# Optimization experiments

Measured on AMD Instinct MI355X. Metric: run time of the kernel, lower is better.

The kernel has to match this reference:

```python
import jax, jax.numpy as jnp
import numpy as np

SR = 44100.0  # sample_rate from init_kwargs


def _alpha(tau_ms):
    # Eq. (10): alpha = exp(-1 / (tau_s * fs)), tau clamped to [0.1, 1000] ms
    tau_s = jnp.clip(tau_ms, 0.1, 1000.0) / 1000.0
    return jnp.exp(-1.0 / (tau_s * SR))


def _env(x, alpha, attack):
    # Nonlinear envelope follower (Eqs. 9-10).
    # attack=True  -> smooth attack (when |x| rising), instant decay
    # attack=False -> smooth decay  (when |x| falling), instant attack
    xa = jnp.abs(x)
    xs = jnp.moveaxis(xa, -1, 0)  # [T, B, C]
    y0 = jnp.zeros(xa.shape[:-1], xa.dtype)  # [B, C]

    def step(y_prev, xn):
        cond = (xn > y_prev) if attack else (xn < y_prev)
        y_curr = jnp.where(cond, (1.0 - alpha) * xn + alpha * y_prev, xn)
        return y_curr, y_curr

    _, ys = jax.lax.scan(step, y0, xs)
    return jnp.moveaxis(ys, 0, -1)  # [B, C, T]


def _db_to_amp(db):
    return jnp.power(10.0, db / 20.0)


def reference(x, tauAtc, tauDtc, nu, dBregDelta):
    # Temporal Contrast Enhancement (Weger et al., ICAD 2019, Eqs. 12-14).
    # high_pass_filter is the identity in the source, so sh = x.
    alpha_d = _alpha(jnp.clip(tauDtc, 1.0, 100.0))
    alpha_a = _alpha(jnp.clip(tauAtc, 1.0, 100.0))
    et_d = _env(x, alpha_d, attack=False)      # envd(sh)
    et_a = _env(et_d, alpha_a, attack=True)    # enva(et_d)
    nu_amp = _db_to_amp(jnp.clip(nu, -60.0, 0.0))
    et = jnp.maximum(et_d - et_a - nu_amp, 0.0)
    et_env = _env(et, alpha_d, attack=False)   # envd(et)
    reg = _db_to_amp(jnp.clip(dBregDelta, -120.0, -60.0))
    modulation = et / (et_env + reg)
    return x * modulation


def setup_inputs() -> dict:
    key = jax.random.key(0)
    x = jax.random.normal(key, (8, 32, 88200), dtype=jnp.float32)  # [B, C, T]
    return {
        "x": x,
        "tauAtc": jnp.float32(3.0),
        "tauDtc": jnp.float32(7.0),
        "nu": jnp.float32(-40.0),
        "dBregDelta": jnp.float32(-96.0),
    }
```

## Files before the change

### kernel.cpp

```cpp
#include <hip/hip_runtime.h>
#include <cmath>


typedef float f32x4 __attribute__((ext_vector_type(4)));

static constexpr int   kT  = 88200;
static constexpr float kSR = 44100.0f;

static constexpr int S       = 40;
static constexpr int NC      = kT / S;
static constexpr int PADS    = S + 4;
static constexpr int CHT     = 256;
static constexpr int NT      = (NC + CHT - 1) / CHT;
static constexpr int TAILC   = NC - CHT * (NT - 1);
static constexpr int F4C     = S / 4;
static constexpr int TILE_F4 = CHT * F4C;
static constexpr int TAIL_F4 = TAILC * F4C;
static constexpr int BUF_F   = CHT * PADS;

struct EnvP { float ad, bd, aa, ba, nuamp, reg; };

__device__ __forceinline__ EnvP make_params(const float* tauA, const float* tauD,
                                            const float* nu, const float* dbreg) {
  EnvP p;
  float td = fminf(fmaxf(tauD[0], 1.0f), 100.0f);
  td = fminf(fmaxf(td, 0.1f), 1000.0f) * 0.001f;
  float ta = fminf(fmaxf(tauA[0], 1.0f), 100.0f);
  ta = fminf(fmaxf(ta, 0.1f), 1000.0f) * 0.001f;
  p.ad = expf(-1.0f / (td * kSR));
  p.aa = expf(-1.0f / (ta * kSR));
  p.bd = 1.0f - p.ad;
  p.ba = 1.0f - p.aa;
  p.nuamp = exp10f(fminf(fmaxf(nu[0],    -60.0f),   0.0f) * 0.05f);
  p.reg   = exp10f(fminf(fmaxf(dbreg[0], -120.0f), -60.0f) * 0.05f);
  return p;
}

template <int MODE>
__device__ __forceinline__ void sweep(const float* __restrict__ xs,
                                      float* __restrict__ os,
                                      const EnvP& p,
                                      float* __restrict__ buf0,
                                      float* __restrict__ buf1,
                                      float* __restrict__ Ac, float* __restrict__ Bc,
                                      const float* __restrict__ Ydl,
                                      const float* __restrict__ Yal,
                                      const float* __restrict__ Yel,
                                      int t) {
  f32x4 r0, r1, r2, r3, r4, r5, r6, r7, r8, r9;
  const f32x4* xg4 = reinterpret_cast<const f32x4*>(xs);

#define LD_TILE(TILE)                                                        \
  do {                                                                       \
    const int nf4_ = ((TILE) == NT - 1) ? TAIL_F4 : TILE_F4;                 \
    const f32x4* xg_ = xg4 + (size_t)(TILE) * TILE_F4;                       \
    int i0_ = t;                                                             \
    r0 = xg_[i0_ < nf4_ ? i0_ : 0];  i0_ += 256;                             \
    r1 = xg_[i0_ < nf4_ ? i0_ : 0];  i0_ += 256;                             \
    r2 = xg_[i0_ < nf4_ ? i0_ : 0];  i0_ += 256;                             \
    r3 = xg_[i0_ < nf4_ ? i0_ : 0];  i0_ += 256;                             \
    r4 = xg_[i0_ < nf4_ ? i0_ : 0];  i0_ += 256;                             \
    r5 = xg_[i0_ < nf4_ ? i0_ : 0];  i0_ += 256;                             \
    r6 = xg_[i0_ < nf4_ ? i0_ : 0];  i0_ += 256;                             \
    r7 = xg_[i0_ < nf4_ ? i0_ : 0];  i0_ += 256;                             \
    r8 = xg_[i0_ < nf4_ ? i0_ : 0];  i0_ += 256;                             \
    r9 = xg_[i0_ < nf4_ ? i0_ : 0];                                          \
  } while (0)

#define WR_TILE(BUF)                                                         \
  do {                                                                       \
    float* b_ = (BUF);                                                       \
    int i0_ = t, ch_, of_;                                                   \
    ch_ = i0_ / F4C; of_ = (i0_ - ch_ * F4C) * 4;                            \
    *reinterpret_cast<f32x4*>(&b_[ch_ * PADS + of_]) = r0;  i0_ += 256;      \
    ch_ = i0_ / F4C; of_ = (i0_ - ch_ * F4C) * 4;                            \
    *reinterpret_cast<f32x4*>(&b_[ch_ * PADS + of_]) = r1;  i0_ += 256;      \
    ch_ = i0_ / F4C; of_ = (i0_ - ch_ * F4C) * 4;                            \
    *reinterpret_cast<f32x4*>(&b_[ch_ * PADS + of_]) = r2;  i0_ += 256;      \
    ch_ = i0_ / F4C; of_ = (i0_ - ch_ * F4C) * 4;                            \
    *reinterpret_cast<f32x4*>(&b_[ch_ * PADS + of_]) = r3;  i0_ += 256;      \
    ch_ = i0_ / F4C; of_ = (i0_ - ch_ * F4C) * 4;                            \
    *reinterpret_cast<f32x4*>(&b_[ch_ * PADS + of_]) = r4;  i0_ += 256;      \
    ch_ = i0_ / F4C; of_ = (i0_ - ch_ * F4C) * 4;                            \
    *reinterpret_cast<f32x4*>(&b_[ch_ * PADS + of_]) = r5;  i0_ += 256;      \
    ch_ = i0_ / F4C; of_ = (i0_ - ch_ * F4C) * 4;                            \
    *reinterpret_cast<f32x4*>(&b_[ch_ * PADS + of_]) = r6;  i0_ += 256;      \
    ch_ = i0_ / F4C; of_ = (i0_ - ch_ * F4C) * 4;                            \
    *reinterpret_cast<f32x4*>(&b_[ch_ * PADS + of_]) = r7;  i0_ += 256;      \
    ch_ = i0_ / F4C; of_ = (i0_ - ch_ * F4C) * 4;                            \
    *reinterpret_cast<f32x4*>(&b_[ch_ * PADS + of_]) = r8;  i0_ += 256;      \
    ch_ = i0_ / F4C; of_ = (i0_ - ch_ * F4C) * 4;                            \
    *reinterpret_cast<f32x4*>(&b_[ch_ * PADS + of_]) = r9;                   \
  } while (0)

  LD_TILE(0);
  WR_TILE(buf0);
  __syncthreads();
  int cur = 0;
  for (int it = 0; it < NT; ++it) {
    const bool pf = (it + 1 < NT);
    if (pf) LD_TILE(it + 1);
    __builtin_amdgcn_sched_barrier(0);
    float* bc = cur ? buf1 : buf0;
    float* bn = cur ? buf0 : buf1;
    const int c = it * CHT + t;
    if (c < NC) {
      float* my = &bc[t * PADS];
      if (MODE == 0) {
        float A = -INFINITY, B = 0.0f;
#pragma unroll 2
        for (int i = 0; i < F4C; ++i) {
          f32x4 v = *reinterpret_cast<const f32x4*>(&my[4 * i]);
#pragma unroll
          for (int j = 0; j < 4; ++j) {
            float xa = fabsf(v[j]);
            float bx = p.bd * xa;
            A = fmaxf(xa, fmaf(p.ad, A, bx));
            B = fmaf(p.ad, B, bx);
          }
        }
        Ac[c] = A; Bc[c] = B;
      } else if (MODE == 1) {
        float yd = Ydl[c];
        float A = INFINITY, B = 0.0f;
#pragma unroll 2
        for (int i = 0; i < F4C; ++i) {
          f32x4 v = *reinterpret_cast<const f32x4*>(&my[4 * i]);
#pragma unroll
          for (int j = 0; j < 4; ++j) {
            float xa = fabsf(v[j]);
            yd = fmaxf(xa, fmaf(p.ad, yd, p.bd * xa));
            float by = p.ba * yd;
            A = fminf(yd, fmaf(p.aa, A, by));
            B = fmaf(p.aa, B, by);
          }
        }
        Ac[c] = A; Bc[c] = B;
      } else if (MODE == 2) {
        float yd = Ydl[c], ya = Yal[c];
        float A = -INFINITY, B = 0.0f;
#pragma unroll 2
        for (int i = 0; i < F4C; ++i) {
          f32x4 v = *reinterpret_cast<const f32x4*>(&my[4 * i]);
#pragma unroll
          for (int j = 0; j < 4; ++j) {
            float xa = fabsf(v[j]);
            yd = fmaxf(xa, fmaf(p.ad, yd, p.bd * xa));
            ya = fminf(yd, fmaf(p.aa, ya, p.ba * yd));
            float et = fmaxf((yd - ya) - p.nuamp, 0.0f);
            float bx = p.bd * et;
            A = fmaxf(et, fmaf(p.ad, A, bx));
            B = fmaf(p.ad, B, bx);
          }
        }
        Ac[c] = A; Bc[c] = B;
      } else {
        float yd = Ydl[c], ya = Yal[c], ye = Yel[c];
#pragma unroll 2
        for (int i = 0; i < F4C; ++i) {
          f32x4 v = *reinterpret_cast<const f32x4*>(&my[4 * i]);
          f32x4 oo;
#pragma unroll
          for (int j = 0; j < 4; ++j) {
            float xa = fabsf(v[j]);
            yd = fmaxf(xa, fmaf(p.ad, yd, p.bd * xa));
            ya = fminf(yd, fmaf(p.aa, ya, p.ba * yd));
            float et = fmaxf((yd - ya) - p.nuamp, 0.0f);
            ye = fmaxf(et, fmaf(p.ad, ye, p.bd * et));
            oo[j] = v[j] * (et / (ye + p.reg));
          }
          *reinterpret_cast<f32x4*>(&my[4 * i]) = oo;
        }
      }
    }
    if (MODE == 3) {
      __syncthreads();
      f32x4* og = reinterpret_cast<f32x4*>(os) + (size_t)it * TILE_F4;
      const int nf4 = pf ? TILE_F4 : TAIL_F4;
#pragma unroll
      for (int i = 0; i < F4C; ++i) {
        int idx = t + i * 256;
        if (idx < nf4) {
          int chunk = idx / F4C;
          int off   = (idx - chunk * F4C) * 4;
          f32x4 v = *reinterpret_cast<const f32x4*>(&bc[chunk * PADS + off]);
          __builtin_nontemporal_store(v, &og[idx]);
        }
      }
    }
    if (pf) WR_TILE(bn);
    __syncthreads();
    cur ^= 1;
  }
#undef LD_TILE
#undef WR_TILE
}

template <int ATTACK>
__device__ __forceinline__ void scan_lds(const float* __restrict__ Ac,
                                         const float* __restrict__ Bc,
                                         float* __restrict__ Y,
                                         const EnvP& p,
                                         float* __restrict__ sbuf, int t) {
  constexpr int CPT = (NC + 255) / 256;
  const float alpha = ATTACK ? p.aa : p.ad;
  const float ID_A  = ATTACK ? INFINITY : -INFINITY;
  const float gS = powf(alpha, (float)S);

  float ca[CPT], cb[CPT];
  float a = ID_A, b = 0.0f, g = 1.0f;
#pragma unroll
  for (int k = 0; k < CPT; ++k) {
    int c = t * CPT + k;
    if (c < NC) { ca[k] = Ac[c]; cb[k] = Bc[c]; }
    else        { ca[k] = ID_A;  cb[k] = 0.0f; }
    float cg = (c < NC) ? gS : 1.0f;
    float na = ATTACK ? fminf(ca[k], fmaf(cg, a, cb[k]))
                      : fmaxf(ca[k], fmaf(cg, a, cb[k]));
    b = fmaf(cg, b, cb[k]);
    g = cg * g;
    a = na;
  }

  float* sA = sbuf; float* sB = sbuf + 256; float* sG = sbuf + 512;
  sA[t] = a; sB[t] = b; sG[t] = g;
  __syncthreads();
#pragma unroll
  for (int d = 1; d < 256; d <<= 1) {
    float pa = 0.0f, pb = 0.0f, pg = 0.0f;
    if (t >= d) { pa = sA[t - d]; pb = sB[t - d]; pg = sG[t - d]; }
    __syncthreads();
    if (t >= d) {
      float na = ATTACK ? fminf(a, fmaf(g, pa, b)) : fmaxf(a, fmaf(g, pa, b));
      b = fmaf(g, pb, b);
      g = g * pg;
      a = na;
      sA[t] = a; sB[t] = b; sG[t] = g;
    }
    __syncthreads();
  }

  float ea, eb;
  if (t == 0) { ea = ID_A; eb = 0.0f; }
  else        { ea = sA[t - 1]; eb = sB[t - 1]; }

#pragma unroll
  for (int k = 0; k < CPT; ++k) {
    int c = t * CPT + k;
    if (c >= NC) break;
    Y[c] = ATTACK ? fminf(ea, eb) : fmaxf(ea, eb);
    float na = ATTACK ? fminf(ca[k], fmaf(gS, ea, cb[k]))
                      : fmaxf(ca[k], fmaf(gS, ea, cb[k]));
    eb = fmaf(gS, eb, cb[k]);
    ea = na;
  }
}

__global__
__attribute__((amdgpu_flat_work_group_size(256, 256), amdgpu_waves_per_eu(1, 1)))
void k_one(const float* __restrict__ x,
           const float* tauA, const float* tauD,
           const float* nu, const float* dbreg,
           float* __restrict__ out) {
  extern __shared__ float lds[];
  float* buf0 = lds;
  float* buf1 = lds + BUF_F;
  float* Ac   = lds + 2 * BUF_F;
  float* Bc   = Ac + NC;
  float* Yd   = Bc + NC;
  float* Ya   = Yd + NC;
  float* Ye   = Ya + NC;
  const int t = threadIdx.x;
  const float* xs = x   + (size_t)blockIdx.x * kT;
  float*       os = out + (size_t)blockIdx.x * kT;
  EnvP p = make_params(tauA, tauD, nu, dbreg);

  sweep<0>(xs, nullptr, p, buf0, buf1, Ac, Bc, nullptr, nullptr, nullptr, t);
  scan_lds<0>(Ac, Bc, Yd, p, buf0, t);
  __syncthreads();
  sweep<1>(xs, nullptr, p, buf0, buf1, Ac, Bc, Yd, nullptr, nullptr, t);
  scan_lds<1>(Ac, Bc, Ya, p, buf0, t);
  __syncthreads();
  sweep<2>(xs, nullptr, p, buf0, buf1, Ac, Bc, Yd, Ya, nullptr, t);
  scan_lds<0>(Ac, Bc, Ye, p, buf0, t);
  __syncthreads();
  sweep<3>(xs, os, p, buf0, buf1, Ac, Bc, Yd, Ya, Ye, t);
}

template <int FS, int MODE>
__global__ __launch_bounds__(256)
void k_pass(const float* __restrict__ x,
            const float* tauA, const float* tauD,
            const float* nu, const float* dbreg,
            const float* __restrict__ FYd, const float* __restrict__ FYa,
            const float* __restrict__ FYe,
            float* __restrict__ O0, float* __restrict__ O1) {
  constexpr int FP = FS + 4;
  __shared__ float lds[256 * FP];
  const int t   = threadIdx.x;
  const int blk = blockIdx.x;
  const size_t tileBase = (size_t)blk * (256 * FS);
  const float4* xg = reinterpret_cast<const float4*>(x + tileBase);
#pragma unroll
  for (int i = 0; i < FS / 4; ++i) {
    int idx = t + i * 256;
    float4 v = xg[idx];
    int chunk = (idx * 4) / FS;
    int off   = idx * 4 - chunk * FS;
    *reinterpret_cast<float4*>(&lds[chunk * FP + off]) = v;
  }
  __syncthreads();
  EnvP p = make_params(tauA, tauD, nu, dbreg);
  const int gchunk = blk * 256 + t;
  float* my = &lds[t * FP];
  if (MODE == 0) {
    float A = -INFINITY, B = 0.0f;
#pragma unroll 2
    for (int i = 0; i < FS / 4; ++i) {
      float4 v = *reinterpret_cast<const float4*>(&my[4 * i]);
      float vv[4] = {v.x, v.y, v.z, v.w};
#pragma unroll
      for (int j = 0; j < 4; ++j) {
        float xa = fabsf(vv[j]);
        float bx = p.bd * xa;
        A = fmaxf(xa, fmaf(p.ad, A, bx));
        B = fmaf(p.ad, B, bx);
      }
    }
    O0[gchunk] = A; O1[gchunk] = B;
  } else if (MODE == 1) {
    float yd = FYd[gchunk];
    float A = INFINITY, B = 0.0f;
#pragma unroll 2
    for (int i = 0; i < FS / 4; ++i) {
      float4 v = *reinterpret_cast<const float4*>(&my[4 * i]);
      float vv[4] = {v.x, v.y, v.z, v.w};
#pragma unroll
      for (int j = 0; j < 4; ++j) {
        float xa = fabsf(vv[j]);
        yd = fmaxf(xa, fmaf(p.ad, yd, p.bd * xa));
        float by = p.ba * yd;
        A = fminf(yd, fmaf(p.aa, A, by));
        B = fmaf(p.aa, B, by);
      }
    }
    O0[gchunk] = A; O1[gchunk] = B;
  } else if (MODE == 2) {
    float yd = FYd[gchunk], ya = FYa[gchunk];
    float A = -INFINITY, B = 0.0f;
#pragma unroll 2
    for (int i = 0; i < FS / 4; ++i) {
      float4 v = *reinterpret_cast<const float4*>(&my[4 * i]);
      float vv[4] = {v.x, v.y, v.z, v.w};
#pragma unroll
      for (int j = 0; j < 4; ++j) {
        float xa = fabsf(vv[j]);
        yd = fmaxf(xa, fmaf(p.ad, yd, p.bd * xa));
        ya = fminf(yd, fmaf(p.aa, ya, p.ba * yd));
        float et = fmaxf((yd - ya) - p.nuamp, 0.0f);
        float bx = p.bd * et;
        A = fmaxf(et, fmaf(p.ad, A, bx));
        B = fmaf(p.ad, B, bx);
      }
    }
    O0[gchunk] = A; O1[gchunk] = B;
  } else {
    float yd = FYd[gchunk], ya = FYa[gchunk], ye = FYe[gchunk];
#pragma unroll 2
    for (int i = 0; i < FS / 4; ++i) {
      float4 v = *reinterpret_cast<const float4*>(&my[4 * i]);
      float vv[4] = {v.x, v.y, v.z, v.w};
      float oo[4];
#pragma unroll
      for (int j = 0; j < 4; ++j) {
        float xa = fabsf(vv[j]);
        yd = fmaxf(xa, fmaf(p.ad, yd, p.bd * xa));
        ya = fminf(yd, fmaf(p.aa, ya, p.ba * yd));
        float et = fmaxf((yd - ya) - p.nuamp, 0.0f);
        ye = fmaxf(et, fmaf(p.ad, ye, p.bd * et));
        oo[j] = vv[j] * (et / (ye + p.reg));
      }
      *reinterpret_cast<float4*>(&my[4 * i]) = make_float4(oo[0], oo[1], oo[2], oo[3]);
    }
    __syncthreads();
    float4* og = reinterpret_cast<float4*>(O0 + tileBase);
#pragma unroll
    for (int i = 0; i < FS / 4; ++i) {
      int idx = t + i * 256;
      int chunk = (idx * 4) / FS;
      int off   = idx * 4 - chunk * FS;
      og[idx] = *reinterpret_cast<const float4*>(&lds[chunk * FP + off]);
    }
  }
}

template <int FS, int ATTACK>
__global__ __launch_bounds__(256)
void k_scan(const float* __restrict__ A, const float* __restrict__ B,
            float* __restrict__ Y,
            const float* tauA, const float* tauD,
            const float* nu, const float* dbreg) {
  constexpr int FNC = kT / FS;
  constexpr int CPT = (FNC + 255) / 256;
  EnvP p = make_params(tauA, tauD, nu, dbreg);
  const float alpha = ATTACK ? p.aa : p.ad;
  const float ID_A  = ATTACK ? INFINITY : -INFINITY;
  int s = blockIdx.x, t = threadIdx.x;
  long base = (long)s * FNC;
  float gS = powf(alpha, (float)FS);

  float ca[CPT], cb[CPT];
  float a = ID_A, b = 0.0f, g = 1.0f;
#pragma unroll
  for (int k = 0; k < CPT; ++k) {
    int c = t * CPT + k;
    if (c < FNC) { ca[k] = A[base + c]; cb[k] = B[base + c]; }
    else         { ca[k] = ID_A;        cb[k] = 0.0f; }
    float cg = (c < FNC) ? gS : 1.0f;
    float na = ATTACK ? fminf(ca[k], fmaf(cg, a, cb[k]))
                      : fmaxf(ca[k], fmaf(cg, a, cb[k]));
    b = fmaf(cg, b, cb[k]);
    g = cg * g;
    a = na;
  }

  __shared__ float sA[256], sB[256], sG[256];
  sA[t] = a; sB[t] = b; sG[t] = g;
  __syncthreads();
#pragma unroll
  for (int d = 1; d < 256; d <<= 1) {
    float pa = 0.0f, pb = 0.0f, pg = 0.0f;
    if (t >= d) { pa = sA[t - d]; pb = sB[t - d]; pg = sG[t - d]; }
    __syncthreads();
    if (t >= d) {
      float na = ATTACK ? fminf(a, fmaf(g, pa, b)) : fmaxf(a, fmaf(g, pa, b));
      b = fmaf(g, pb, b);
      g = g * pg;
      a = na;
      sA[t] = a; sB[t] = b; sG[t] = g;
    }
    __syncthreads();
  }

  float ea, eb;
  if (t == 0) { ea = ID_A; eb = 0.0f; }
  else        { ea = sA[t - 1]; eb = sB[t - 1]; }

#pragma unroll
  for (int k = 0; k < CPT; ++k) {
    int c = t * CPT + k;
    if (c >= FNC) break;
    Y[base + c] = ATTACK ? fminf(ea, eb) : fmaxf(ea, eb);
    float na = ATTACK ? fminf(ca[k], fmaf(gS, ea, cb[k]))
                      : fmaxf(ca[k], fmaf(gS, ea, cb[k]));
    eb = fmaf(gS, eb, cb[k]);
    ea = na;
  }
}

template <int FS>
static void run_pipeline(const float* x, const float* tauA, const float* tauD,
                         const float* nu, const float* dbreg, float* out,
                         float* wsf, int nseries, hipStream_t stream) {
  const int nc  = kT / FS;
  const int nch = nseries * nc;
  float* A   = wsf;
  float* B   = wsf + (size_t)nch;
  float* FYd = wsf + (size_t)2 * nch;
  float* FYa = wsf + (size_t)3 * nch;
  float* FYe = wsf + (size_t)4 * nch;
  const int grid = nch / 256;

  k_pass<FS, 0><<<grid, 256, 0, stream>>>(x, tauA, tauD, nu, dbreg, nullptr, nullptr, nullptr, A, B);
  k_scan<FS, 0><<<nseries, 256, 0, stream>>>(A, B, FYd, tauA, tauD, nu, dbreg);
  k_pass<FS, 1><<<grid, 256, 0, stream>>>(x, tauA, tauD, nu, dbreg, FYd, nullptr, nullptr, A, B);
  k_scan<FS, 1><<<nseries, 256, 0, stream>>>(A, B, FYa, tauA, tauD, nu, dbreg);
  k_pass<FS, 2><<<grid, 256, 0, stream>>>(x, tauA, tauD, nu, dbreg, FYd, FYa, nullptr, A, B);
  k_scan<FS, 0><<<nseries, 256, 0, stream>>>(A, B, FYe, tauA, tauD, nu, dbreg);
  k_pass<FS, 3><<<grid, 256, 0, stream>>>(x, tauA, tauD, nu, dbreg, FYd, FYa, FYe, out, nullptr);
}

extern "C" void kernel_launch(void* const* d_in, const int* in_sizes, int n_in,
                              void* d_out, int out_size, void* d_ws, size_t ws_size,
                              hipStream_t stream) {
  const float* x     = (const float*)d_in[0];
  const float* tauA  = (const float*)d_in[1];
  const float* tauD  = (const float*)d_in[2];
  const float* nu    = (const float*)d_in[3];
  const float* dbreg = (const float*)d_in[4];
  float* out = (float*)d_out;
  float* wsf = (float*)d_ws;
  const int nseries = in_sizes[0] / kT;

  constexpr size_t LDSZ = (size_t)(2 * BUF_F + 5 * NC) * sizeof(float);

  static int fusedOK = -1;
  if (fusedOK < 0) {
    hipFuncSetAttribute(reinterpret_cast<const void*>(&k_one),
                        hipFuncAttributeMaxDynamicSharedMemorySize, (int)LDSZ);
    (void)hipGetLastError();
    fusedOK = 1;
  }

  if (fusedOK == 1) {
    k_one<<<nseries, 256, LDSZ, stream>>>(x, tauA, tauD, nu, dbreg, out);
    if (hipGetLastError() == hipSuccess) return;
    fusedOK = 0;
  }

  auto fits = [&](int FS) {
    return (size_t)5 * nseries * (kT / FS) * sizeof(float) <= ws_size;
  };
  if      (fits(40))  run_pipeline<40 >(x, tauA, tauD, nu, dbreg, out, wsf, nseries, stream);
  else if (fits(56))  run_pipeline<56 >(x, tauA, tauD, nu, dbreg, out, wsf, nseries, stream);
  else if (fits(72))  run_pipeline<72 >(x, tauA, tauD, nu, dbreg, out, wsf, nseries, stream);
  else                run_pipeline<120>(x, tauA, tauD, nu, dbreg, out, wsf, nseries, stream);
}
```

Measured before the change: 219.0 us.

## Use 512-thread blocks with 24-sample chunks and move carry arrays to global

```diff
diff --git a/kernel.cpp b/kernel.cpp
--- a/kernel.cpp
+++ b/kernel.cpp
@@ -7,16 +7,16 @@
 static constexpr int   kT  = 88200;
 static constexpr float kSR = 44100.0f;
 
-static constexpr int S       = 40;
-static constexpr int NC      = kT / S;
-static constexpr int PADS    = S + 4;
-static constexpr int CHT     = 256;
-static constexpr int NT      = (NC + CHT - 1) / CHT;
-static constexpr int TAILC   = NC - CHT * (NT - 1);
-static constexpr int F4C     = S / 4;
-static constexpr int TILE_F4 = CHT * F4C;
-static constexpr int TAIL_F4 = TAILC * F4C;
-static constexpr int BUF_F   = CHT * PADS;
+static constexpr int FS_      = 24;
+static constexpr int FNC_     = kT / FS_;
+static constexpr int FPADS    = FS_ + 4;
+static constexpr int FTH      = 512;
+static constexpr int FNT      = (FNC_ + FTH - 1) / FTH;
+static constexpr int FTAILC   = FNC_ - FTH * (FNT - 1);
+static constexpr int FF4C     = FS_ / 4;
+static constexpr int FTILE_F4 = FTH * FF4C;
+static constexpr int FTAIL_F4 = FTAILC * FF4C;
+static constexpr int FBUF_F   = FTH * FPADS;
 
 struct EnvP { float ad, bd, aa, ba, nuamp, reg; };
 
@@ -47,69 +47,57 @@
                                       const float* __restrict__ Yal,
                                       const float* __restrict__ Yel,
                                       int t) {
-  f32x4 r0, r1, r2, r3, r4, r5, r6, r7, r8, r9;
+  f32x4 r0, r1, r2, r3, r4, r5;
   const f32x4* xg4 = reinterpret_cast<const f32x4*>(xs);
 
 #define LD_TILE(TILE)                                                        \
   do {                                                                       \
-    const int nf4_ = ((TILE) == NT - 1) ? TAIL_F4 : TILE_F4;                 \
-    const f32x4* xg_ = xg4 + (size_t)(TILE) * TILE_F4;                       \
+    const int nf4_ = ((TILE) == FNT - 1) ? FTAIL_F4 : FTILE_F4;              \
+    const f32x4* xg_ = xg4 + (size_t)(TILE) * FTILE_F4;                      \
     int i0_ = t;                                                             \
-    r0 = xg_[i0_ < nf4_ ? i0_ : 0];  i0_ += 256;                             \
-    r1 = xg_[i0_ < nf4_ ? i0_ : 0];  i0_ += 256;                             \
-    r2 = xg_[i0_ < nf4_ ? i0_ : 0];  i0_ += 256;                             \
-    r3 = xg_[i0_ < nf4_ ? i0_ : 0];  i0_ += 256;                             \
-    r4 = xg_[i0_ < nf4_ ? i0_ : 0];  i0_ += 256;                             \
-    r5 = xg_[i0_ < nf4_ ? i0_ : 0];  i0_ += 256;                             \
-    r6 = xg_[i0_ < nf4_ ? i0_ : 0];  i0_ += 256;                             \
-    r7 = xg_[i0_ < nf4_ ? i0_ : 0];  i0_ += 256;                             \
-    r8 = xg_[i0_ < nf4_ ? i0_ : 0];  i0_ += 256;                             \
-    r9 = xg_[i0_ < nf4_ ? i0_ : 0];                                          \
+    r0 = xg_[i0_ < nf4_ ? i0_ : 0];  i0_ += FTH;                             \
+    r1 = xg_[i0_ < nf4_ ? i0_ : 0];  i0_ += FTH;                             \
+    r2 = xg_[i0_ < nf4_ ? i0_ : 0];  i0_ += FTH;                             \
+    r3 = xg_[i0_ < nf4_ ? i0_ : 0];  i0_ += FTH;                             \
+    r4 = xg_[i0_ < nf4_ ? i0_ : 0];  i0_ += FTH;                             \
+    r5 = xg_[i0_ < nf4_ ? i0_ : 0];                                          \
   } while (0)
 
 #define WR_TILE(BUF)                                                         \
   do {                                                                       \
     float* b_ = (BUF);                                                       \
     int i0_ = t, ch_, of_;                                                   \
-    ch_ = i0_ / F4C; of_ = (i0_ - ch_ * F4C) * 4;                            \
-    *reinterpret_cast<f32x4*>(&b_[ch_ * PADS + of_]) = r0;  i0_ += 256;      \
-    ch_ = i0_ / F4C; of_ = (i0_ - ch_ * F4C) * 4;                            \
-    *reinterpret_cast<f32x4*>(&b_[ch_ * PADS + of_]) = r1;  i0_ += 256;      \
-    ch_ = i0_ / F4C; of_ = (i0_ - ch_ * F4C) * 4;                            \
-    *reinterpret_cast<f32x4*>(&b_[ch_ * PADS + of_]) = r2;  i0_ += 256;      \
-    ch_ = i0_ / F4C; of_ = (i0_ - ch_ * F4C) * 4;                            \
-    *reinterpret_cast<f32x4*>(&b_[ch_ * PADS + of_]) = r3;  i0_ += 256;      \
-    ch_ = i0_ / F4C; of_ = (i0_ - ch_ * F4C) * 4;                            \
-    *reinterpret_cast<f32x4*>(&b_[ch_ * PADS + of_]) = r4;  i0_ += 256;      \
-    ch_ = i0_ / F4C; of_ = (i0_ - ch_ * F4C) * 4;                            \
-    *reinterpret_cast<f32x4*>(&b_[ch_ * PADS + of_]) = r5;  i0_ += 256;      \
-    ch_ = i0_ / F4C; of_ = (i0_ - ch_ * F4C) * 4;                            \
-    *reinterpret_cast<f32x4*>(&b_[ch_ * PADS + of_]) = r6;  i0_ += 256;      \
-    ch_ = i0_ / F4C; of_ = (i0_ - ch_ * F4C) * 4;                            \
-    *reinterpret_cast<f32x4*>(&b_[ch_ * PADS + of_]) = r7;  i0_ += 256;      \
-    ch_ = i0_ / F4C; of_ = (i0_ - ch_ * F4C) * 4;                            \
-    *reinterpret_cast<f32x4*>(&b_[ch_ * PADS + of_]) = r8;  i0_ += 256;      \
-    ch_ = i0_ / F4C; of_ = (i0_ - ch_ * F4C) * 4;                            \
-    *reinterpret_cast<f32x4*>(&b_[ch_ * PADS + of_]) = r9;                   \
+    ch_ = i0_ / FF4C; of_ = (i0_ - ch_ * FF4C) * 4;                          \
+    *reinterpret_cast<f32x4*>(&b_[ch_ * FPADS + of_]) = r0;  i0_ += FTH;     \
+    ch_ = i0_ / FF4C; of_ = (i0_ - ch_ * FF4C) * 4;                          \
+    *reinterpret_cast<f32x4*>(&b_[ch_ * FPADS + of_]) = r1;  i0_ += FTH;     \
+    ch_ = i0_ / FF4C; of_ = (i0_ - ch_ * FF4C) * 4;                          \
+    *reinterpret_cast<f32x4*>(&b_[ch_ * FPADS + of_]) = r2;  i0_ += FTH;     \
+    ch_ = i0_ / FF4C; of_ = (i0_ - ch_ * FF4C) * 4;                          \
+    *reinterpret_cast<f32x4*>(&b_[ch_ * FPADS + of_]) = r3;  i0_ += FTH;     \
+    ch_ = i0_ / FF4C; of_ = (i0_ - ch_ * FF4C) * 4;                          \
+    *reinterpret_cast<f32x4*>(&b_[ch_ * FPADS + of_]) = r4;  i0_ += FTH;     \
+    ch_ = i0_ / FF4C; of_ = (i0_ - ch_ * FF4C) * 4;                          \
+    *reinterpret_cast<f32x4*>(&b_[ch_ * FPADS + of_]) = r5;                  \
   } while (0)
 
   LD_TILE(0);
   WR_TILE(buf0);
   __syncthreads();
   int cur = 0;
-  for (int it = 0; it < NT; ++it) {
-    const bool pf = (it + 1 < NT);
+  for (int it = 0; it < FNT; ++it) {
+    const bool pf = (it + 1 < FNT);
     if (pf) LD_TILE(it + 1);
     __builtin_amdgcn_sched_barrier(0);
     float* bc = cur ? buf1 : buf0;
     float* bn = cur ? buf0 : buf1;
-    const int c = it * CHT + t;
-    if (c < NC) {
-      float* my = &bc[t * PADS];
+    const int c = it * FTH + t;
+    if (c < FNC_) {
+      float* my = &bc[t * FPADS];
       if (MODE == 0) {
         float A = -INFINITY, B = 0.0f;
 #pragma unroll 2
-        for (int i = 0; i < F4C; ++i) {
+        for (int i = 0; i < FF4C; ++i) {
           f32x4 v = *reinterpret_cast<const f32x4*>(&my[4 * i]);
 #pragma unroll
           for (int j = 0; j < 4; ++j) {
@@ -124,7 +112,7 @@
         float yd = Ydl[c];
         float A = INFINITY, B = 0.0f;
 #pragma unroll 2
-        for (int i = 0; i < F4C; ++i) {
+        for (int i = 0; i < FF4C; ++i) {
           f32x4 v = *reinterpret_cast<const f32x4*>(&my[4 * i]);
 #pragma unroll
           for (int j = 0; j < 4; ++j) {
@@ -140,7 +128,7 @@
         float yd = Ydl[c], ya = Yal[c];
         float A = -INFINITY, B = 0.0f;
 #pragma unroll 2
-        for (int i = 0; i < F4C; ++i) {
+        for (int i = 0; i < FF4C; ++i) {
           f32x4 v = *reinterpret_cast<const f32x4*>(&my[4 * i]);
 #pragma unroll
           for (int j = 0; j < 4; ++j) {
@@ -157,7 +145,7 @@
       } else {
         float yd = Ydl[c], ya = Yal[c], ye = Yel[c];
 #pragma unroll 2
-        for (int i = 0; i < F4C; ++i) {
+        for (int i = 0; i < FF4C; ++i) {
           f32x4 v = *reinterpret_cast<const f32x4*>(&my[4 * i]);
           f32x4 oo;
 #pragma unroll
@@ -175,15 +163,15 @@
     }
     if (MODE == 3) {
       __syncthreads();
-      f32x4* og = reinterpret_cast<f32x4*>(os) + (size_t)it * TILE_F4;
-      const int nf4 = pf ? TILE_F4 : TAIL_F4;
-#pragma unroll
-      for (int i = 0; i < F4C; ++i) {
-        int idx = t + i * 256;
+      f32x4* og = reinterpret_cast<f32x4*>(os) + (size_t)it * FTILE_F4;
+      const int nf4 = pf ? FTILE_F4 : FTAIL_F4;
+#pragma unroll
+      for (int i = 0; i < FF4C; ++i) {
+        int idx = t + i * FTH;
         if (idx < nf4) {
-          int chunk = idx / F4C;
-          int off   = (idx - chunk * F4C) * 4;
-          f32x4 v = *reinterpret_cast<const f32x4*>(&bc[chunk * PADS + off]);
+          int chunk = idx / FF4C;
+          int off   = (idx - chunk * FF4C) * 4;
+          f32x4 v = *reinterpret_cast<const f32x4*>(&bc[chunk * FPADS + off]);
           __builtin_nontemporal_store(v, &og[idx]);
         }
       }
@@ -202,19 +190,19 @@
                                          float* __restrict__ Y,
                                          const EnvP& p,
                                          float* __restrict__ sbuf, int t) {
-  constexpr int CPT = (NC + 255) / 256;
+  constexpr int CPT = (FNC_ + FTH - 1) / FTH;
   const float alpha = ATTACK ? p.aa : p.ad;
   const float ID_A  = ATTACK ? INFINITY : -INFINITY;
-  const float gS = powf(alpha, (float)S);
+  const float gS = powf(alpha, (float)FS_);
 
   float ca[CPT], cb[CPT];
   float a = ID_A, b = 0.0f, g = 1.0f;
 #pragma unroll
   for (int k = 0; k < CPT; ++k) {
     int c = t * CPT + k;
-    if (c < NC) { ca[k] = Ac[c]; cb[k] = Bc[c]; }
-    else        { ca[k] = ID_A;  cb[k] = 0.0f; }
-    float cg = (c < NC) ? gS : 1.0f;
+    if (c < FNC_) { ca[k] = Ac[c]; cb[k] = Bc[c]; }
+    else          { ca[k] = ID_A;  cb[k] = 0.0f; }
+    float cg = (c < FNC_) ? gS : 1.0f;
     float na = ATTACK ? fminf(ca[k], fmaf(cg, a, cb[k]))
                       : fmaxf(ca[k], fmaf(cg, a, cb[k]));
     b = fmaf(cg, b, cb[k]);
@@ -222,11 +210,11 @@
     a = na;
   }
 
-  float* sA = sbuf; float* sB = sbuf + 256; float* sG = sbuf + 512;
+  float* sA = sbuf; float* sB = sbuf + FTH; float* sG = sbuf + 2 * FTH;
   sA[t] = a; sB[t] = b; sG[t] = g;
   __syncthreads();
 #pragma unroll
-  for (int d = 1; d < 256; d <<= 1) {
+  for (int d = 1; d < FTH; d <<= 1) {
     float pa = 0.0f, pb = 0.0f, pg = 0.0f;
     if (t >= d) { pa = sA[t - d]; pb = sB[t - d]; pg = sG[t - d]; }
     __syncthreads();
@@ -247,7 +235,7 @@
 #pragma unroll
   for (int k = 0; k < CPT; ++k) {
     int c = t * CPT + k;
-    if (c >= NC) break;
+    if (c >= FNC_) break;
     Y[c] = ATTACK ? fminf(ea, eb) : fmaxf(ea, eb);
     float na = ATTACK ? fminf(ca[k], fmaf(gS, ea, cb[k]))
                       : fmaxf(ca[k], fmaf(gS, ea, cb[k]));
@@ -257,22 +245,25 @@
 }
 
 __global__
-__attribute__((amdgpu_flat_work_group_size(256, 256), amdgpu_waves_per_eu(1, 1)))
+__attribute__((amdgpu_flat_work_group_size(512, 512), amdgpu_waves_per_eu(2, 2)))
 void k_one(const float* __restrict__ x,
            const float* tauA, const float* tauD,
            const float* nu, const float* dbreg,
+           float* __restrict__ Ydg, float* __restrict__ Yag,
+           float* __restrict__ Yeg,
            float* __restrict__ out) {
   extern __shared__ float lds[];
   float* buf0 = lds;
-  float* buf1 = lds + BUF_F;
-  float* Ac   = lds + 2 * BUF_F;
-  float* Bc   = Ac + NC;
-  float* Yd   = Bc + NC;
-  float* Ya   = Yd + NC;
-  float* Ye   = Ya + NC;
+  float* buf1 = lds + FBUF_F;
+  float* Ac   = lds + 2 * FBUF_F;
+  float* Bc   = Ac + FNC_;
   const int t = threadIdx.x;
-  const float* xs = x   + (size_t)blockIdx.x * kT;
-  float*       os = out + (size_t)blockIdx.x * kT;
+  const int s = blockIdx.x;
+  const float* xs = x   + (size_t)s * kT;
+  float*       os = out + (size_t)s * kT;
+  float* Yd = Ydg + (size_t)s * FNC_;
+  float* Ya = Yag + (size_t)s * FNC_;
+  float* Ye = Yeg + (size_t)s * FNC_;
   EnvP p = make_params(tauA, tauD, nu, dbreg);
 
   sweep<0>(xs, nullptr, p, buf0, buf1, Ac, Bc, nullptr, nullptr, nullptr, t);
@@ -492,7 +483,9 @@
   float* wsf = (float*)d_ws;
   const int nseries = in_sizes[0] / kT;
 
-  constexpr size_t LDSZ = (size_t)(2 * BUF_F + 5 * NC) * sizeof(float);
+  constexpr size_t LDSZ = (size_t)(2 * FBUF_F + 2 * FNC_) * sizeof(float);
+  const size_t NS = (size_t)FNC_ * nseries;
+  const bool wsOK = 3 * NS * sizeof(float) <= ws_size;
 
   static int fusedOK = -1;
   if (fusedOK < 0) {
@@ -502,8 +495,11 @@
     fusedOK = 1;
   }
 
-  if (fusedOK == 1) {
-    k_one<<<nseries, 256, LDSZ, stream>>>(x, tauA, tauD, nu, dbreg, out);
+  if (fusedOK == 1 && wsOK) {
+    float* Yd = wsf;
+    float* Ya = wsf + NS;
+    float* Ye = wsf + 2 * NS;
+    k_one<<<nseries, FTH, LDSZ, stream>>>(x, tauA, tauD, nu, dbreg, Yd, Ya, Ye, out);
     if (hipGetLastError() == hipSuccess) return;
     fusedOK = 0;
   }
```

Result: slower. 226.8 us (+3.6%).
